# Performance work log

Hardware: AMD Instinct MI355X
Metric: run time of the kernel (lower is better)

Reference implementation:

```python
import jax, jax.numpy as jnp
import numpy as np

B, T, C, FREQ = 32, 512, 22, 192
HID = 128


def setup_inputs() -> dict:
    key = jax.random.key(0)
    k1, k2, k3, k4, k5, k6 = jax.random.split(key, 6)
    x = jax.random.normal(k1, (B, T, C, FREQ), dtype=jnp.float32)
    A = jax.random.uniform(k2, (B, T, C, C), dtype=jnp.float32)
    # Linear weights (torch layout: [out, in]); scaled like torch default init
    W0 = jax.random.normal(k3, (HID, FREQ), dtype=jnp.float32) / np.sqrt(FREQ)
    b0 = jax.random.normal(k4, (HID,), dtype=jnp.float32) * 0.01
    W1 = jax.random.normal(k5, (HID, HID), dtype=jnp.float32) / np.sqrt(HID)
    b1 = jax.random.normal(k6, (HID,), dtype=jnp.float32) * 0.01
    return {"x": x, "A": A, "W0": W0, "b0": b0, "W1": W1, "b1": b1}


def reference(x, A, W0, b0, W1, b1):
    # Vectorized over B and T simultaneously (original python-loops over t).
    # Layer i: xt = relu(Linear(bmm(A_t, xt)))
    h = x  # [B,T,C,Freq]
    for W, b in ((W0, b0), (W1, b1)):
        h = jnp.einsum('btij,btjf->btif', A, h)          # adjacency mix over nodes
        h = jax.nn.relu(jnp.einsum('btcf,hf->btch', h, W) + b)  # Linear + ReLU
    # stack over t is implicit; mean over node dim C -> [B,T,HID]
    return h.mean(axis=2)
```

## Files before the change

kernel.cpp:

```cpp
#include <hip/hip_runtime.h>

#define CC 22
#define FF 192
#define HH 128
#define NBT (32 * 512)

typedef __attribute__((ext_vector_type(8))) __bf16 bf16x8;
typedef __attribute__((ext_vector_type(8))) short s16x8;
typedef __attribute__((ext_vector_type(4))) float f32x4;

__device__ __forceinline__ float bf2f(unsigned short u) {
    union { unsigned int i; float f; } v;
    v.i = ((unsigned int)u) << 16;
    return v.f;
}

__device__ __forceinline__ unsigned short f2bf(float f) {
    union { float f; unsigned int i; } v;
    v.f = f;
    return (unsigned short)((v.i + 0x7fffu + ((v.i >> 16) & 1u)) >> 16);
}

__device__ __forceinline__ void split2(float v, unsigned short& h, unsigned short& l) {
    h = f2bf(v);
    float r = v - bf2f(h);
    l = f2bf(r);
}

__device__ __forceinline__ unsigned int cvt_pk_bf16(float a, float b) {
    unsigned int r;
    asm("v_cvt_pk_bf16_f32 %0, %1, %2" : "=v"(r) : "v"(a), "v"(b));
    return r;
}

__device__ __forceinline__ void split_pk2(float a, float b,
                                          unsigned int& hi, unsigned int& lo) {
    hi = cvt_pk_bf16(a, b);
    union { unsigned int i; float f; } ha, hb;
    ha.i = hi << 16;
    hb.i = hi & 0xffff0000u;
    lo = cvt_pk_bf16(a - ha.f, b - hb.f);
}

__device__ __forceinline__ bf16x8 bzero8() {
    s16x8 z = {0, 0, 0, 0, 0, 0, 0, 0};
    return __builtin_bit_cast(bf16x8, z);
}

__device__ __forceinline__ int ybyte(int row, int b) {
    return row * 64 + (b ^ (((row >> 1) & 3) << 4));
}

__device__ __forceinline__ int inputs_are_bf16(const unsigned short* __restrict__ A,
                                               int tid) {
    const float v = bf2f(A[tid & 63]);
    return __all(v >= 0.0f && v <= 1.0001f);
}

#define WS0H 0
#define WS0L 24576
#define WS1H 49152
#define WS1L 65536

__global__ void convert_weights(const float* __restrict__ W0g,
                                const float* __restrict__ W1g,
                                const unsigned short* __restrict__ Aany,
                                unsigned short* __restrict__ wsW) {
    if (inputs_are_bf16(Aany, threadIdx.x)) return;
    const int i = blockIdx.x * 256 + threadIdx.x;
    if (i < HH * FF) {
        unsigned short h, l;
        split2(W0g[i], h, l);
        wsW[WS0H + i] = h;
        wsW[WS0L + i] = l;
    } else {
        const int j = i - HH * FF;
        if (j < HH * HH) {
            unsigned short h, l;
            split2(W1g[j], h, l);
            wsW[WS1H + j] = h;
            wsW[WS1L + j] = l;
        }
    }
}

__device__ void run_block_f32(
    const float* __restrict__ xg, const float* __restrict__ Ag,
    const float* __restrict__ W0g, const float* __restrict__ b0g,
    const float* __restrict__ W1g, const float* __restrict__ b1g,
    float* __restrict__ outg, int bt, int tid,
    float* sA, float* sX, float* sH1)
{
    float* sH2  = sX;
    float* sH3  = sH1;
    float* sRed = sA;

    const float* Ap = Ag + (size_t)bt * (CC * CC);
    for (int i = tid; i < CC * CC; i += 256) sA[i] = Ap[i];
    const float4* xp = (const float4*)(xg + (size_t)bt * (CC * FF));
    for (int i = tid; i < CC * FF / 4; i += 256) ((float4*)sX)[i] = xp[i];
    __syncthreads();

    for (int idx4 = tid; idx4 < CC * FF / 4; idx4 += 256) {
        const int c  = idx4 / (FF / 4);
        const int fq = idx4 - c * (FF / 4);
        float4 acc = make_float4(0.f, 0.f, 0.f, 0.f);
        #pragma unroll
        for (int j = 0; j < CC; ++j) {
            const float  a  = sA[c * CC + j];
            const float4 xv = *(const float4*)&sX[j * FF + 4 * fq];
            acc.x += a * xv.x; acc.y += a * xv.y;
            acc.z += a * xv.z; acc.w += a * xv.w;
        }
        ((float4*)sH1)[idx4] = acc;
    }
    __syncthreads();

    const int h  = tid & 127;
    const int ty = tid >> 7;

    {
        float acc[11];
        const float bb = b0g[h];
        #pragma unroll
        for (int i = 0; i < 11; ++i) acc[i] = bb;
        #pragma unroll 4
        for (int fq = 0; fq < FF / 4; ++fq) {
            float4 u = ((const float4*)(W0g + h * FF))[fq];
            #pragma unroll
            for (int i = 0; i < 11; ++i) {
                const float4 xv = *(const float4*)&sH1[(2 * i + ty) * FF + 4 * fq];
                acc[i] = fmaf(xv.x, u.x, fmaf(xv.y, u.y, fmaf(xv.z, u.z, fmaf(xv.w, u.w, acc[i]))));
            }
        }
        #pragma unroll
        for (int i = 0; i < 11; ++i)
            sH2[(2 * i + ty) * HH + h] = fmaxf(acc[i], 0.f);
    }
    __syncthreads();

    for (int idx4 = tid; idx4 < CC * HH / 4; idx4 += 256) {
        const int c  = idx4 / (HH / 4);
        const int kq = idx4 - c * (HH / 4);
        float4 acc = make_float4(0.f, 0.f, 0.f, 0.f);
        #pragma unroll
        for (int j = 0; j < CC; ++j) {
            const float  a  = sA[c * CC + j];
            const float4 xv = *(const float4*)&sH2[j * HH + 4 * kq];
            acc.x += a * xv.x; acc.y += a * xv.y;
            acc.z += a * xv.z; acc.w += a * xv.w;
        }
        ((float4*)sH3)[idx4] = acc;
    }
    __syncthreads();

    {
        float acc[11];
        const float bb = b1g[h];
        #pragma unroll
        for (int i = 0; i < 11; ++i) acc[i] = bb;
        #pragma unroll 4
        for (int kq = 0; kq < HH / 4; ++kq) {
            float4 u = ((const float4*)(W1g + h * HH))[kq];
            #pragma unroll
            for (int i = 0; i < 11; ++i) {
                const float4 xv = *(const float4*)&sH3[(2 * i + ty) * HH + 4 * kq];
                acc[i] = fmaf(xv.x, u.x, fmaf(xv.y, u.y, fmaf(xv.z, u.z, fmaf(xv.w, u.w, acc[i]))));
            }
        }
        float s = 0.f;
        #pragma unroll
        for (int i = 0; i < 11; ++i) s += fmaxf(acc[i], 0.f);
        sRed[ty * HH + h] = s;
    }
    __syncthreads();

    if (ty == 0) {
        const float m = (sRed[h] + sRed[HH + h]) * (1.0f / 22.0f);
        outg[(size_t)bt * HH + h] = m;
    }
}

__device__ void run_block_split(
    const float* __restrict__ xg, const float* __restrict__ Ag,
    const float* __restrict__ b0g, const float* __restrict__ b1g,
    const unsigned short* __restrict__ wsW,
    float* __restrict__ outg, int bt, int tid, char* smem)
{
    unsigned short* sxh  = (unsigned short*)smem;
    unsigned short* sxl  = (unsigned short*)(smem + 8800);
    unsigned short* sAh  = (unsigned short*)(smem + 17600);
    unsigned short* sAl  = (unsigned short*)(smem + 20160);
    char*           syh  = smem + 22720;
    char*           syl  = smem + 30912;
    unsigned short* sh3h = (unsigned short*)smem;
    unsigned short* sh3l = (unsigned short*)(smem + 8704);

    const unsigned short* W0h = wsW + WS0H;
    const unsigned short* W0l = wsW + WS0L;
    const unsigned short* W1h = wsW + WS1H;
    const unsigned short* W1l = wsW + WS1L;

    {
        const float4* xp4 = (const float4*)(xg + (size_t)bt * (CC * FF));
        for (int idx = tid; idx < CC * (FF / 4); idx += 256) {
            const int c = idx / (FF / 4);
            const int q = idx - c * (FF / 4);
            const float4 v = xp4[idx];
            uint2 hv, lv;
            split_pk2(v.x, v.y, hv.x, lv.x);
            split_pk2(v.z, v.w, hv.y, lv.y);
            *(uint2*)&sxh[c * 200 + 4 * q] = hv;
            *(uint2*)&sxl[c * 200 + 4 * q] = lv;
        }
        const float* Ap = Ag + (size_t)bt * (CC * CC);
        for (int idx = tid; idx < 32 * 40; idx += 256) {
            const int r = idx / 40;
            const int c = idx - r * 40;
            unsigned short h = 0, l = 0;
            if (r < CC && c < CC) split2(Ap[r * CC + c], h, l);
            sAh[idx] = h;
            sAl[idx] = l;
        }
    }
    __syncthreads();

    const int lane = tid & 63;
    const int wid  = tid >> 6;
    const int lr   = lane & 15;
    const int lk   = lane >> 4;
    const int hb   = wid * 32;

    const f32x4 vzero = {0.f, 0.f, 0.f, 0.f};

    {
        f32x4 acc[2][2];
        #pragma unroll
        for (int mt = 0; mt < 2; ++mt)
            #pragma unroll
            for (int nt = 0; nt < 2; ++nt) acc[mt][nt] = vzero;

        #pragma unroll
        for (int ks = 0; ks < 6; ++ks) {
            bf16x8 xfh[2], xfl[2];
            #pragma unroll
            for (int mt = 0; mt < 2; ++mt) {
                const int row = mt * 16 + lr;
                const int rr  = (row < CC) ? row : 0;
                const int off = rr * 200 + ks * 32 + lk * 8;
                bf16x8 fh = *(const bf16x8*)(sxh + off);
                bf16x8 fl = *(const bf16x8*)(sxl + off);
                if (row >= CC) { fh = bzero8(); fl = bzero8(); }
                xfh[mt] = fh; xfl[mt] = fl;
            }
            bf16x8 wfh[2], wfl[2];
            #pragma unroll
            for (int nt = 0; nt < 2; ++nt) {
                const int hcol = hb + nt * 16 + lr;
                const int off  = hcol * FF + ks * 32 + lk * 8;
                wfh[nt] = *(const bf16x8*)(W0h + off);
                wfl[nt] = *(const bf16x8*)(W0l + off);
            }
            #pragma unroll
            for (int mt = 0; mt < 2; ++mt)
                #pragma unroll
                for (int nt = 0; nt < 2; ++nt) {
                    acc[mt][nt] = __builtin_amdgcn_mfma_f32_16x16x32_bf16(xfh[mt], wfh[nt], acc[mt][nt], 0, 0, 0);
                    acc[mt][nt] = __builtin_amdgcn_mfma_f32_16x16x32_bf16(xfl[mt], wfh[nt], acc[mt][nt], 0, 0, 0);
                    acc[mt][nt] = __builtin_amdgcn_mfma_f32_16x16x32_bf16(xfh[mt], wfl[nt], acc[mt][nt], 0, 0, 0);
                }
        }
        #pragma unroll
        for (int mt = 0; mt < 2; ++mt)
            #pragma unroll
            for (int nt = 0; nt < 2; ++nt) {
                const int hcol = hb + nt * 16 + lr;
                uint2 hv, lv;
                split_pk2(acc[mt][nt][0], acc[mt][nt][1], hv.x, lv.x);
                split_pk2(acc[mt][nt][2], acc[mt][nt][3], hv.y, lv.y);
                const int boff = ybyte(hcol, mt * 32 + lk * 8);
                *(uint2*)(syh + boff) = hv;
                *(uint2*)(syl + boff) = lv;
            }
    }
    __syncthreads();

    bf16x8 Afh[2], Afl[2];
    #pragma unroll
    for (int t = 0; t < 2; ++t) {
        const int off = (t * 16 + lr) * 40 + lk * 8;
        Afh[t] = *(const bf16x8*)(sAh + off);
        Afl[t] = *(const bf16x8*)(sAl + off);
    }

    {
        f32x4 acc[2][2];
        #pragma unroll
        for (int nt = 0; nt < 2; ++nt) {
            const float b = b0g[hb + nt * 16 + lr];
            const f32x4 bv = {b, b, b, b};
            acc[0][nt] = bv;
            acc[1][nt] = bv;
        }
        bf16x8 yfh[2], yfl[2];
        #pragma unroll
        for (int nt = 0; nt < 2; ++nt) {
            const int boff = ybyte(hb + nt * 16 + lr, lk * 16);
            yfh[nt] = *(const bf16x8*)(syh + boff);
            yfl[nt] = *(const bf16x8*)(syl + boff);
        }
        asm volatile("" ::: "memory");
        #pragma unroll
        for (int mt = 0; mt < 2; ++mt)
            #pragma unroll
            for (int nt = 0; nt < 2; ++nt) {
                acc[mt][nt] = __builtin_amdgcn_mfma_f32_16x16x32_bf16(Afh[mt], yfh[nt], acc[mt][nt], 0, 0, 0);
                acc[mt][nt] = __builtin_amdgcn_mfma_f32_16x16x32_bf16(Afl[mt], yfh[nt], acc[mt][nt], 0, 0, 0);
                acc[mt][nt] = __builtin_amdgcn_mfma_f32_16x16x32_bf16(Afh[mt], yfl[nt], acc[mt][nt], 0, 0, 0);
            }
        #pragma unroll
        for (int mt = 0; mt < 2; ++mt)
            #pragma unroll
            for (int nt = 0; nt < 2; ++nt) {
                const int hcol = hb + nt * 16 + lr;
                uint2 hv, lv;
                split_pk2(fmaxf(acc[mt][nt][0], 0.f), fmaxf(acc[mt][nt][1], 0.f), hv.x, lv.x);
                split_pk2(fmaxf(acc[mt][nt][2], 0.f), fmaxf(acc[mt][nt][3], 0.f), hv.y, lv.y);
                const int boff = ybyte(hcol, mt * 32 + lk * 8);
                *(uint2*)(syh + boff) = hv;
                *(uint2*)(syl + boff) = lv;
            }
    }

    {
        f32x4 acc[2][2];
        #pragma unroll
        for (int mt = 0; mt < 2; ++mt)
            #pragma unroll
            for (int ct = 0; ct < 2; ++ct) acc[mt][ct] = vzero;

        bf16x8 gfh[2], gfl[2];
        #pragma unroll
        for (int mt = 0; mt < 2; ++mt) {
            const int boff = ybyte(hb + mt * 16 + lr, lk * 16);
            gfh[mt] = *(const bf16x8*)(syh + boff);
            gfl[mt] = *(const bf16x8*)(syl + boff);
        }
        #pragma unroll
        for (int mt = 0; mt < 2; ++mt)
            #pragma unroll
            for (int ct = 0; ct < 2; ++ct) {
                acc[mt][ct] = __builtin_amdgcn_mfma_f32_16x16x32_bf16(gfh[mt], Afh[ct], acc[mt][ct], 0, 0, 0);
                acc[mt][ct] = __builtin_amdgcn_mfma_f32_16x16x32_bf16(gfl[mt], Afh[ct], acc[mt][ct], 0, 0, 0);
                acc[mt][ct] = __builtin_amdgcn_mfma_f32_16x16x32_bf16(gfh[mt], Afl[ct], acc[mt][ct], 0, 0, 0);
            }
        #pragma unroll
        for (int mt = 0; mt < 2; ++mt)
            #pragma unroll
            for (int ct = 0; ct < 2; ++ct) {
                const int cp = ct * 16 + lr;
                uint2 hv, lv;
                split_pk2(acc[mt][ct][0], acc[mt][ct][1], hv.x, lv.x);
                split_pk2(acc[mt][ct][2], acc[mt][ct][3], hv.y, lv.y);
                const int e = cp * 136 + hb + mt * 16 + lk * 4;
                *(uint2*)&sh3h[e] = hv;
                *(uint2*)&sh3l[e] = lv;
            }
    }
    __syncthreads();

    {
        f32x4 acc[2][2];
        #pragma unroll
        for (int mt = 0; mt < 2; ++mt) {
            const float4 bv = *(const float4*)(b1g + hb + mt * 16 + lk * 4);
            const f32x4 bb = {bv.x, bv.y, bv.z, bv.w};
            acc[mt][0] = bb;
            acc[mt][1] = bb;
        }
        #pragma unroll
        for (int ks = 0; ks < 4; ++ks) {
            bf16x8 wfh[2], wfl[2], hfh[2], hfl[2];
            #pragma unroll
            for (int mt = 0; mt < 2; ++mt) {
                const int o   = hb + mt * 16 + lr;
                const int off = o * HH + ks * 32 + lk * 8;
                wfh[mt] = *(const bf16x8*)(W1h + off);
                wfl[mt] = *(const bf16x8*)(W1l + off);
            }
            #pragma unroll
            for (int ct = 0; ct < 2; ++ct) {
                const int off = (ct * 16 + lr) * 136 + ks * 32 + lk * 8;
                hfh[ct] = *(const bf16x8*)(sh3h + off);
                hfl[ct] = *(const bf16x8*)(sh3l + off);
            }
            #pragma unroll
            for (int mt = 0; mt < 2; ++mt)
                #pragma unroll
                for (int ct = 0; ct < 2; ++ct) {
                    acc[mt][ct] = __builtin_amdgcn_mfma_f32_16x16x32_bf16(wfh[mt], hfh[ct], acc[mt][ct], 0, 0, 0);
                    acc[mt][ct] = __builtin_amdgcn_mfma_f32_16x16x32_bf16(wfl[mt], hfh[ct], acc[mt][ct], 0, 0, 0);
                    acc[mt][ct] = __builtin_amdgcn_mfma_f32_16x16x32_bf16(wfh[mt], hfl[ct], acc[mt][ct], 0, 0, 0);
                }
        }
        float s[2][4];
        #pragma unroll
        for (int mt = 0; mt < 2; ++mt)
            #pragma unroll
            for (int r = 0; r < 4; ++r) {
                float v = fmaxf(acc[mt][0][r], 0.f);
                if (lr < CC - 16) v += fmaxf(acc[mt][1][r], 0.f);
                s[mt][r] = v;
            }
        #pragma unroll
        for (int m = 1; m < 16; m <<= 1)
            #pragma unroll
            for (int mt = 0; mt < 2; ++mt)
                #pragma unroll
                for (int r = 0; r < 4; ++r)
                    s[mt][r] += __shfl_xor(s[mt][r], m);

        if (lr == 0) {
            const float inv = 1.0f / 22.0f;
            #pragma unroll
            for (int mt = 0; mt < 2; ++mt) {
                float4 o4;
                o4.x = s[mt][0] * inv;
                o4.y = s[mt][1] * inv;
                o4.z = s[mt][2] * inv;
                o4.w = s[mt][3] * inv;
                *(float4*)(outg + (size_t)bt * HH + hb + mt * 16 + lk * 4) = o4;
            }
        }
    }
}

__device__ void run_block_bf16(
    const unsigned short* __restrict__ xg, const unsigned short* __restrict__ Ag,
    const unsigned short* __restrict__ W0g, const unsigned short* __restrict__ b0g,
    const unsigned short* __restrict__ W1g, const unsigned short* __restrict__ b1g,
    unsigned short* __restrict__ outg, int bt, int tid, char* smem)
{
    unsigned short* sXT  = (unsigned short*)smem;
    unsigned short* sAm  = (unsigned short*)(smem + 15360);
    unsigned short* sH1  = (unsigned short*)(smem + 17920);
    unsigned short* sH2T = (unsigned short*)smem;
    unsigned short* sH3  = (unsigned short*)(smem + 17920);

    const unsigned short* xp = xg + (size_t)bt * (CC * FF);
    const unsigned short* Ap = Ag + (size_t)bt * (CC * CC);

    for (int id = tid; id < 32 * 40; id += 256) {
        const int r = id / 40;
        const int c = id - r * 40;
        sAm[id] = (r < CC && c < CC) ? Ap[r * CC + c] : (unsigned short)0;
    }
    for (int id = tid; id < FF * 9; id += 256) {
        const int f = id / 9;
        const int q = id - f * 9;
        ((unsigned int*)sXT)[f * 20 + 11 + q] = 0u;
    }
    for (int id = tid; id < 24 * CC; id += 256) {
        const int fb = id / CC;
        const int j  = id - fb * CC;
        const uint4 v = *(const uint4*)(xp + j * FF + fb * 8);
        unsigned short* d = sXT + (fb * 8) * 40 + j;
        d[0 * 40] = (unsigned short)(v.x & 0xffffu);
        d[1 * 40] = (unsigned short)(v.x >> 16);
        d[2 * 40] = (unsigned short)(v.y & 0xffffu);
        d[3 * 40] = (unsigned short)(v.y >> 16);
        d[4 * 40] = (unsigned short)(v.z & 0xffffu);
        d[5 * 40] = (unsigned short)(v.z >> 16);
        d[6 * 40] = (unsigned short)(v.w & 0xffffu);
        d[7 * 40] = (unsigned short)(v.w >> 16);
    }
    __syncthreads();

    const int lane = tid & 63;
    const int wid  = tid >> 6;
    const int lr   = lane & 15;
    const int lk   = lane >> 4;
    const f32x4 vzero = {0.f, 0.f, 0.f, 0.f};

    {
        f32x4 acc[3][2];
        #pragma unroll
        for (int i = 0; i < 3; ++i)
            #pragma unroll
            for (int j = 0; j < 2; ++j) acc[i][j] = vzero;
        bf16x8 xa[3], ab[2];
        #pragma unroll
        for (int i = 0; i < 3; ++i)
            xa[i] = *(const bf16x8*)(sXT + ((3 * wid + i) * 16 + lr) * 40 + lk * 8);
        #pragma unroll
        for (int j = 0; j < 2; ++j)
            ab[j] = *(const bf16x8*)(sAm + (j * 16 + lr) * 40 + lk * 8);
        #pragma unroll
        for (int i = 0; i < 3; ++i)
            #pragma unroll
            for (int j = 0; j < 2; ++j)
                acc[i][j] = __builtin_amdgcn_mfma_f32_16x16x32_bf16(xa[i], ab[j], acc[i][j], 0, 0, 0);
        #pragma unroll
        for (int i = 0; i < 3; ++i) {
            const int fbase = (3 * wid + i) * 16 + lk * 4;
            #pragma unroll
            for (int j = 0; j < 2; ++j) {
                const int c = j * 16 + lr;
                ushort4 st;
                st.x = f2bf(acc[i][j][0]);
                st.y = f2bf(acc[i][j][1]);
                st.z = f2bf(acc[i][j][2]);
                st.w = f2bf(acc[i][j][3]);
                *(ushort4*)(sH1 + c * 200 + fbase) = st;
            }
        }
    }
    __syncthreads();

    {
        f32x4 acc[2][2];
        #pragma unroll
        for (int nt = 0; nt < 2; ++nt) {
            const float bv = bf2f(b0g[(2 * wid + nt) * 16 + lr]);
            f32x4 bvv = {bv, bv, bv, bv};
            acc[0][nt] = bvv;
            acc[1][nt] = bvv;
        }
        #pragma unroll
        for (int ks = 0; ks < 6; ++ks) {
            bf16x8 af[2], bfr[2];
            #pragma unroll
            for (int mt = 0; mt < 2; ++mt)
                af[mt] = *(const bf16x8*)(sH1 + (mt * 16 + lr) * 200 + ks * 32 + lk * 8);
            #pragma unroll
            for (int nt = 0; nt < 2; ++nt)
                bfr[nt] = *(const bf16x8*)(W0g + ((size_t)((2 * wid + nt) * 16 + lr)) * FF + ks * 32 + lk * 8);
            #pragma unroll
            for (int mt = 0; mt < 2; ++mt)
                #pragma unroll
                for (int nt = 0; nt < 2; ++nt)
                    acc[mt][nt] = __builtin_amdgcn_mfma_f32_16x16x32_bf16(af[mt], bfr[nt], acc[mt][nt], 0, 0, 0);
        }
        #pragma unroll
        for (int mt = 0; mt < 2; ++mt) {
            const int cbase = mt * 16 + lk * 4;
            #pragma unroll
            for (int nt = 0; nt < 2; ++nt) {
                const int hcol = (2 * wid + nt) * 16 + lr;
                ushort4 st;
                st.x = (cbase + 0 < CC) ? f2bf(fmaxf(acc[mt][nt][0], 0.f)) : (unsigned short)0;
                st.y = (cbase + 1 < CC) ? f2bf(fmaxf(acc[mt][nt][1], 0.f)) : (unsigned short)0;
                st.z = (cbase + 2 < CC) ? f2bf(fmaxf(acc[mt][nt][2], 0.f)) : (unsigned short)0;
                st.w = (cbase + 3 < CC) ? f2bf(fmaxf(acc[mt][nt][3], 0.f)) : (unsigned short)0;
                *(ushort4*)(sH2T + hcol * 40 + cbase) = st;
            }
        }
    }
    __syncthreads();

    {
        f32x4 acc[2][2];
        #pragma unroll
        for (int mt = 0; mt < 2; ++mt)
            #pragma unroll
            for (int ct = 0; ct < 2; ++ct) acc[mt][ct] = vzero;
        bf16x8 af[2], bb[2];
        #pragma unroll
        for (int mt = 0; mt < 2; ++mt)
            af[mt] = *(const bf16x8*)(sH2T + ((2 * wid + mt) * 16 + lr) * 40 + lk * 8);
        #pragma unroll
        for (int ct = 0; ct < 2; ++ct)
            bb[ct] = *(const bf16x8*)(sAm + (ct * 16 + lr) * 40 + lk * 8);
        #pragma unroll
        for (int mt = 0; mt < 2; ++mt)
            #pragma unroll
            for (int ct = 0; ct < 2; ++ct)
                acc[mt][ct] = __builtin_amdgcn_mfma_f32_16x16x32_bf16(af[mt], bb[ct], acc[mt][ct], 0, 0, 0);
        __syncthreads();
        #pragma unroll
        for (int mt = 0; mt < 2; ++mt) {
            const int hbase = (2 * wid + mt) * 16 + lk * 4;
            #pragma unroll
            for (int ct = 0; ct < 2; ++ct) {
                const int c = ct * 16 + lr;
                ushort4 st;
                st.x = f2bf(acc[mt][ct][0]);
                st.y = f2bf(acc[mt][ct][1]);
                st.z = f2bf(acc[mt][ct][2]);
                st.w = f2bf(acc[mt][ct][3]);
                *(ushort4*)(sH3 + c * 136 + hbase) = st;
            }
        }
    }
    __syncthreads();

    {
        f32x4 acc[2][2];
        #pragma unroll
        for (int mt = 0; mt < 2; ++mt) {
            const ushort4 bu = *(const ushort4*)(b1g + (2 * wid + mt) * 16 + lk * 4);
            f32x4 bvv = {bf2f(bu.x), bf2f(bu.y), bf2f(bu.z), bf2f(bu.w)};
            acc[mt][0] = bvv;
            acc[mt][1] = bvv;
        }
        #pragma unroll
        for (int ks = 0; ks < 4; ++ks) {
            bf16x8 af[2], bfr[2];
            #pragma unroll
            for (int mt = 0; mt < 2; ++mt)
                af[mt] = *(const bf16x8*)(W1g + ((size_t)((2 * wid + mt) * 16 + lr)) * HH + ks * 32 + lk * 8);
            #pragma unroll
            for (int ct = 0; ct < 2; ++ct)
                bfr[ct] = *(const bf16x8*)(sH3 + (ct * 16 + lr) * 136 + ks * 32 + lk * 8);
            #pragma unroll
            for (int mt = 0; mt < 2; ++mt)
                #pragma unroll
                for (int ct = 0; ct < 2; ++ct)
                    acc[mt][ct] = __builtin_amdgcn_mfma_f32_16x16x32_bf16(af[mt], bfr[ct], acc[mt][ct], 0, 0, 0);
        }
        float s[2][4];
        #pragma unroll
        for (int mt = 0; mt < 2; ++mt)
            #pragma unroll
            for (int r = 0; r < 4; ++r) {
                float v = fmaxf(acc[mt][0][r], 0.f);
                if (lr < CC - 16) v += fmaxf(acc[mt][1][r], 0.f);
                s[mt][r] = v;
            }
        #pragma unroll
        for (int m = 1; m < 16; m <<= 1)
            #pragma unroll
            for (int mt = 0; mt < 2; ++mt)
                #pragma unroll
                for (int r = 0; r < 4; ++r)
                    s[mt][r] += __shfl_xor(s[mt][r], m);
        if (lr == 0) {
            const float inv = 1.0f / 22.0f;
            #pragma unroll
            for (int mt = 0; mt < 2; ++mt) {
                ushort4 st;
                st.x = f2bf(s[mt][0] * inv);
                st.y = f2bf(s[mt][1] * inv);
                st.z = f2bf(s[mt][2] * inv);
                st.w = f2bf(s[mt][3] * inv);
                *(ushort4*)(outg + (size_t)bt * HH + (2 * wid + mt) * 16 + lk * 4) = st;
            }
        }
    }
}

__global__ __launch_bounds__(256) void tgcn_kernel(
    const void* __restrict__ x, const void* __restrict__ A,
    const void* __restrict__ W0, const void* __restrict__ b0,
    const void* __restrict__ W1, const void* __restrict__ b1,
    void* __restrict__ out, const unsigned short* __restrict__ wsW,
    int use_split)
{
    __shared__ __align__(16) char smem[39104];

    const int tid = threadIdx.x;
    const int bt  = blockIdx.x;
    const int isbf = inputs_are_bf16((const unsigned short*)A, tid);

    if (isbf) {
        run_block_bf16((const unsigned short*)x, (const unsigned short*)A,
                       (const unsigned short*)W0, (const unsigned short*)b0,
                       (const unsigned short*)W1, (const unsigned short*)b1,
                       (unsigned short*)out, bt, tid, smem);
    } else if (use_split) {
        run_block_split((const float*)x, (const float*)A,
                        (const float*)b0, (const float*)b1,
                        wsW, (float*)out, bt, tid, smem);
    } else {
        float* sA  = (float*)smem;
        float* sX  = (float*)(smem + 1936);
        float* sH1 = (float*)(smem + 18832);
        run_block_f32((const float*)x, (const float*)A,
                      (const float*)W0, (const float*)b0,
                      (const float*)W1, (const float*)b1,
                      (float*)out, bt, tid, sA, sX, sH1);
    }
}

extern "C" void kernel_launch(void* const* d_in, const int* in_sizes, int n_in,
                              void* d_out, int out_size, void* d_ws, size_t ws_size,
                              hipStream_t stream) {
    unsigned short* wsW = (unsigned short*)d_ws;
    const int use_split = (ws_size >= (size_t)(81920 * 2)) ? 1 : 0;

    if (use_split)
        convert_weights<<<160, 256, 0, stream>>>(
            (const float*)d_in[2], (const float*)d_in[4],
            (const unsigned short*)d_in[1], wsW);
    tgcn_kernel<<<NBT, 256, 0, stream>>>(
        d_in[0], d_in[1], d_in[2], d_in[3], d_in[4], d_in[5], d_out,
        wsW, use_split);
}
```

Before: 701.7 us.

## Reorder to project features first, split fp32 inputs in registers, drop weight prepass

The fp32 split path now loads x and the weights straight from global memory and splits them into bf16 hi/lo pairs in registers. This removes the shared-memory staging of x and the separate weight-conversion kernel and workspace. The bf16 path is reordered to apply W0 before the adjacency mix (A(xW)=(Ax)W), which shrinks the first mix from 192 to 128 features and removes the transposed x staging. Shared memory per block drops, which may raise occupancy. In exchange, every block repeats the weight split arithmetic and reads uncoalesced fp32 weights from global memory, and the reordering changes rounding.

Result: slower. 722.8 us (+3.0%).

```diff
diff --git a/kernel.cpp b/kernel.cpp
--- a/kernel.cpp
+++ b/kernel.cpp
@@ -42,6 +42,19 @@
     lo = cvt_pk_bf16(a - ha.f, b - hb.f);
 }
 
+__device__ __forceinline__ void load_split8(const float* __restrict__ p,
+                                            bf16x8& fh, bf16x8& fl) {
+    const float4 a = *(const float4*)p;
+    const float4 b = *(const float4*)(p + 4);
+    uint4 h, l;
+    split_pk2(a.x, a.y, h.x, l.x);
+    split_pk2(a.z, a.w, h.y, l.y);
+    split_pk2(b.x, b.y, h.z, l.z);
+    split_pk2(b.z, b.w, h.w, l.w);
+    fh = __builtin_bit_cast(bf16x8, h);
+    fl = __builtin_bit_cast(bf16x8, l);
+}
+
 __device__ __forceinline__ bf16x8 bzero8() {
     s16x8 z = {0, 0, 0, 0, 0, 0, 0, 0};
     return __builtin_bit_cast(bf16x8, z);
@@ -57,162 +70,20 @@
     return __all(v >= 0.0f && v <= 1.0001f);
 }
 
-#define WS0H 0
-#define WS0L 24576
-#define WS1H 49152
-#define WS1L 65536
-
-__global__ void convert_weights(const float* __restrict__ W0g,
-                                const float* __restrict__ W1g,
-                                const unsigned short* __restrict__ Aany,
-                                unsigned short* __restrict__ wsW) {
-    if (inputs_are_bf16(Aany, threadIdx.x)) return;
-    const int i = blockIdx.x * 256 + threadIdx.x;
-    if (i < HH * FF) {
-        unsigned short h, l;
-        split2(W0g[i], h, l);
-        wsW[WS0H + i] = h;
-        wsW[WS0L + i] = l;
-    } else {
-        const int j = i - HH * FF;
-        if (j < HH * HH) {
-            unsigned short h, l;
-            split2(W1g[j], h, l);
-            wsW[WS1H + j] = h;
-            wsW[WS1L + j] = l;
-        }
-    }
-}
-
-__device__ void run_block_f32(
+__device__ void run_block_split(
     const float* __restrict__ xg, const float* __restrict__ Ag,
     const float* __restrict__ W0g, const float* __restrict__ b0g,
     const float* __restrict__ W1g, const float* __restrict__ b1g,
-    float* __restrict__ outg, int bt, int tid,
-    float* sA, float* sX, float* sH1)
-{
-    float* sH2  = sX;
-    float* sH3  = sH1;
-    float* sRed = sA;
-
-    const float* Ap = Ag + (size_t)bt * (CC * CC);
-    for (int i = tid; i < CC * CC; i += 256) sA[i] = Ap[i];
-    const float4* xp = (const float4*)(xg + (size_t)bt * (CC * FF));
-    for (int i = tid; i < CC * FF / 4; i += 256) ((float4*)sX)[i] = xp[i];
-    __syncthreads();
-
-    for (int idx4 = tid; idx4 < CC * FF / 4; idx4 += 256) {
-        const int c  = idx4 / (FF / 4);
-        const int fq = idx4 - c * (FF / 4);
-        float4 acc = make_float4(0.f, 0.f, 0.f, 0.f);
-        #pragma unroll
-        for (int j = 0; j < CC; ++j) {
-            const float  a  = sA[c * CC + j];
-            const float4 xv = *(const float4*)&sX[j * FF + 4 * fq];
-            acc.x += a * xv.x; acc.y += a * xv.y;
-            acc.z += a * xv.z; acc.w += a * xv.w;
-        }
-        ((float4*)sH1)[idx4] = acc;
-    }
-    __syncthreads();
-
-    const int h  = tid & 127;
-    const int ty = tid >> 7;
-
-    {
-        float acc[11];
-        const float bb = b0g[h];
-        #pragma unroll
-        for (int i = 0; i < 11; ++i) acc[i] = bb;
-        #pragma unroll 4
-        for (int fq = 0; fq < FF / 4; ++fq) {
-            float4 u = ((const float4*)(W0g + h * FF))[fq];
-            #pragma unroll
-            for (int i = 0; i < 11; ++i) {
-                const float4 xv = *(const float4*)&sH1[(2 * i + ty) * FF + 4 * fq];
-                acc[i] = fmaf(xv.x, u.x, fmaf(xv.y, u.y, fmaf(xv.z, u.z, fmaf(xv.w, u.w, acc[i]))));
-            }
-        }
-        #pragma unroll
-        for (int i = 0; i < 11; ++i)
-            sH2[(2 * i + ty) * HH + h] = fmaxf(acc[i], 0.f);
-    }
-    __syncthreads();
-
-    for (int idx4 = tid; idx4 < CC * HH / 4; idx4 += 256) {
-        const int c  = idx4 / (HH / 4);
-        const int kq = idx4 - c * (HH / 4);
-        float4 acc = make_float4(0.f, 0.f, 0.f, 0.f);
-        #pragma unroll
-        for (int j = 0; j < CC; ++j) {
-            const float  a  = sA[c * CC + j];
-            const float4 xv = *(const float4*)&sH2[j * HH + 4 * kq];
-            acc.x += a * xv.x; acc.y += a * xv.y;
-            acc.z += a * xv.z; acc.w += a * xv.w;
-        }
-        ((float4*)sH3)[idx4] = acc;
-    }
-    __syncthreads();
-
-    {
-        float acc[11];
-        const float bb = b1g[h];
-        #pragma unroll
-        for (int i = 0; i < 11; ++i) acc[i] = bb;
-        #pragma unroll 4
-        for (int kq = 0; kq < HH / 4; ++kq) {
-            float4 u = ((const float4*)(W1g + h * HH))[kq];
-            #pragma unroll
-            for (int i = 0; i < 11; ++i) {
-                const float4 xv = *(const float4*)&sH3[(2 * i + ty) * HH + 4 * kq];
-                acc[i] = fmaf(xv.x, u.x, fmaf(xv.y, u.y, fmaf(xv.z, u.z, fmaf(xv.w, u.w, acc[i]))));
-            }
-        }
-        float s = 0.f;
-        #pragma unroll
-        for (int i = 0; i < 11; ++i) s += fmaxf(acc[i], 0.f);
-        sRed[ty * HH + h] = s;
-    }
-    __syncthreads();
-
-    if (ty == 0) {
-        const float m = (sRed[h] + sRed[HH + h]) * (1.0f / 22.0f);
-        outg[(size_t)bt * HH + h] = m;
-    }
-}
-
-__device__ void run_block_split(
-    const float* __restrict__ xg, const float* __restrict__ Ag,
-    const float* __restrict__ b0g, const float* __restrict__ b1g,
-    const unsigned short* __restrict__ wsW,
     float* __restrict__ outg, int bt, int tid, char* smem)
 {
-    unsigned short* sxh  = (unsigned short*)smem;
-    unsigned short* sxl  = (unsigned short*)(smem + 8800);
-    unsigned short* sAh  = (unsigned short*)(smem + 17600);
-    unsigned short* sAl  = (unsigned short*)(smem + 20160);
-    char*           syh  = smem + 22720;
-    char*           syl  = smem + 30912;
+    unsigned short* sAh  = (unsigned short*)smem;
+    unsigned short* sAl  = (unsigned short*)(smem + 2560);
+    char*           syh  = smem + 5120;
+    char*           syl  = smem + 13312;
     unsigned short* sh3h = (unsigned short*)smem;
     unsigned short* sh3l = (unsigned short*)(smem + 8704);
 
-    const unsigned short* W0h = wsW + WS0H;
-    const unsigned short* W0l = wsW + WS0L;
-    const unsigned short* W1h = wsW + WS1H;
-    const unsigned short* W1l = wsW + WS1L;
-
-    {
-        const float4* xp4 = (const float4*)(xg + (size_t)bt * (CC * FF));
-        for (int idx = tid; idx < CC * (FF / 4); idx += 256) {
-            const int c = idx / (FF / 4);
-            const int q = idx - c * (FF / 4);
-            const float4 v = xp4[idx];
-            uint2 hv, lv;
-            split_pk2(v.x, v.y, hv.x, lv.x);
-            split_pk2(v.z, v.w, hv.y, lv.y);
-            *(uint2*)&sxh[c * 200 + 4 * q] = hv;
-            *(uint2*)&sxl[c * 200 + 4 * q] = lv;
-        }
+    {
         const float* Ap = Ag + (size_t)bt * (CC * CC);
         for (int idx = tid; idx < 32 * 40; idx += 256) {
             const int r = idx / 40;
@@ -233,7 +104,16 @@
 
     const f32x4 vzero = {0.f, 0.f, 0.f, 0.f};
 
-    {
+    bf16x8 Afh[2], Afl[2];
+    #pragma unroll
+    for (int t = 0; t < 2; ++t) {
+        const int off = (t * 16 + lr) * 40 + lk * 8;
+        Afh[t] = *(const bf16x8*)(sAh + off);
+        Afl[t] = *(const bf16x8*)(sAl + off);
+    }
+
+    {
+        const float* xb = xg + (size_t)bt * (CC * FF);
         f32x4 acc[2][2];
         #pragma unroll
         for (int mt = 0; mt < 2; ++mt)
@@ -247,9 +127,8 @@
             for (int mt = 0; mt < 2; ++mt) {
                 const int row = mt * 16 + lr;
                 const int rr  = (row < CC) ? row : 0;
-                const int off = rr * 200 + ks * 32 + lk * 8;
-                bf16x8 fh = *(const bf16x8*)(sxh + off);
-                bf16x8 fl = *(const bf16x8*)(sxl + off);
+                bf16x8 fh, fl;
+                load_split8(xb + rr * FF + ks * 32 + lk * 8, fh, fl);
                 if (row >= CC) { fh = bzero8(); fl = bzero8(); }
                 xfh[mt] = fh; xfl[mt] = fl;
             }
@@ -257,9 +136,7 @@
             #pragma unroll
             for (int nt = 0; nt < 2; ++nt) {
                 const int hcol = hb + nt * 16 + lr;
-                const int off  = hcol * FF + ks * 32 + lk * 8;
-                wfh[nt] = *(const bf16x8*)(W0h + off);
-                wfl[nt] = *(const bf16x8*)(W0l + off);
+                load_split8(W0g + hcol * FF + ks * 32 + lk * 8, wfh[nt], wfl[nt]);
             }
             #pragma unroll
             for (int mt = 0; mt < 2; ++mt)
@@ -283,15 +160,6 @@
                 *(uint2*)(syl + boff) = lv;
             }
     }
-    __syncthreads();
-
-    bf16x8 Afh[2], Afl[2];
-    #pragma unroll
-    for (int t = 0; t < 2; ++t) {
-        const int off = (t * 16 + lr) * 40 + lk * 8;
-        Afh[t] = *(const bf16x8*)(sAh + off);
-        Afl[t] = *(const bf16x8*)(sAl + off);
-    }
 
     {
         f32x4 acc[2][2];
@@ -354,6 +222,7 @@
                 acc[mt][ct] = __builtin_amdgcn_mfma_f32_16x16x32_bf16(gfl[mt], Afh[ct], acc[mt][ct], 0, 0, 0);
                 acc[mt][ct] = __builtin_amdgcn_mfma_f32_16x16x32_bf16(gfh[mt], Afl[ct], acc[mt][ct], 0, 0, 0);
             }
+        __syncthreads();
         #pragma unroll
         for (int mt = 0; mt < 2; ++mt)
             #pragma unroll
@@ -383,10 +252,8 @@
             bf16x8 wfh[2], wfl[2], hfh[2], hfl[2];
             #pragma unroll
             for (int mt = 0; mt < 2; ++mt) {
-                const int o   = hb + mt * 16 + lr;
-                const int off = o * HH + ks * 32 + lk * 8;
-                wfh[mt] = *(const bf16x8*)(W1h + off);
-                wfl[mt] = *(const bf16x8*)(W1l + off);
+                const int o = hb + mt * 16 + lr;
+                load_split8(W1g + o * HH + ks * 32 + lk * 8, wfh[mt], wfl[mt]);
             }
             #pragma unroll
             for (int ct = 0; ct < 2; ++ct) {
@@ -441,38 +308,17 @@
     const unsigned short* __restrict__ W1g, const unsigned short* __restrict__ b1g,
     unsigned short* __restrict__ outg, int bt, int tid, char* smem)
 {
-    unsigned short* sXT  = (unsigned short*)smem;
-    unsigned short* sAm  = (unsigned short*)(smem + 15360);
-    unsigned short* sH1  = (unsigned short*)(smem + 17920);
-    unsigned short* sH2T = (unsigned short*)smem;
-    unsigned short* sH3  = (unsigned short*)(smem + 17920);
-
-    const unsigned short* xp = xg + (size_t)bt * (CC * FF);
-    const unsigned short* Ap = Ag + (size_t)bt * (CC * CC);
-
-    for (int id = tid; id < 32 * 40; id += 256) {
-        const int r = id / 40;
-        const int c = id - r * 40;
-        sAm[id] = (r < CC && c < CC) ? Ap[r * CC + c] : (unsigned short)0;
-    }
-    for (int id = tid; id < FF * 9; id += 256) {
-        const int f = id / 9;
-        const int q = id - f * 9;
-        ((unsigned int*)sXT)[f * 20 + 11 + q] = 0u;
-    }
-    for (int id = tid; id < 24 * CC; id += 256) {
-        const int fb = id / CC;
-        const int j  = id - fb * CC;
-        const uint4 v = *(const uint4*)(xp + j * FF + fb * 8);
-        unsigned short* d = sXT + (fb * 8) * 40 + j;
-        d[0 * 40] = (unsigned short)(v.x & 0xffffu);
-        d[1 * 40] = (unsigned short)(v.x >> 16);
-        d[2 * 40] = (unsigned short)(v.y & 0xffffu);
-        d[3 * 40] = (unsigned short)(v.y >> 16);
-        d[4 * 40] = (unsigned short)(v.z & 0xffffu);
-        d[5 * 40] = (unsigned short)(v.z >> 16);
-        d[6 * 40] = (unsigned short)(v.w & 0xffffu);
-        d[7 * 40] = (unsigned short)(v.w >> 16);
+    unsigned short* sAm = (unsigned short*)smem;
+    char*           sy  = smem + 2560;
+    unsigned short* sh3 = (unsigned short*)smem;
+
+    {
+        const unsigned short* Ap = Ag + (size_t)bt * (CC * CC);
+        for (int idx = tid; idx < 32 * 40; idx += 256) {
+            const int r = idx / 40;
+            const int c = idx - r * 40;
+            sAm[idx] = (r < CC && c < CC) ? Ap[r * CC + c] : (unsigned short)0;
+        }
     }
     __syncthreads();
 
@@ -480,143 +326,136 @@
     const int wid  = tid >> 6;
     const int lr   = lane & 15;
     const int lk   = lane >> 4;
+    const int hb   = wid * 32;
     const f32x4 vzero = {0.f, 0.f, 0.f, 0.f};
 
-    {
-        f32x4 acc[3][2];
-        #pragma unroll
-        for (int i = 0; i < 3; ++i)
-            #pragma unroll
-            for (int j = 0; j < 2; ++j) acc[i][j] = vzero;
-        bf16x8 xa[3], ab[2];
-        #pragma unroll
-        for (int i = 0; i < 3; ++i)
-            xa[i] = *(const bf16x8*)(sXT + ((3 * wid + i) * 16 + lr) * 40 + lk * 8);
-        #pragma unroll
-        for (int j = 0; j < 2; ++j)
-            ab[j] = *(const bf16x8*)(sAm + (j * 16 + lr) * 40 + lk * 8);
-        #pragma unroll
-        for (int i = 0; i < 3; ++i)
-            #pragma unroll
-            for (int j = 0; j < 2; ++j)
-                acc[i][j] = __builtin_amdgcn_mfma_f32_16x16x32_bf16(xa[i], ab[j], acc[i][j], 0, 0, 0);
-        #pragma unroll
-        for (int i = 0; i < 3; ++i) {
-            const int fbase = (3 * wid + i) * 16 + lk * 4;
-            #pragma unroll
-            for (int j = 0; j < 2; ++j) {
-                const int c = j * 16 + lr;
-                ushort4 st;
-                st.x = f2bf(acc[i][j][0]);
-                st.y = f2bf(acc[i][j][1]);
-                st.z = f2bf(acc[i][j][2]);
-                st.w = f2bf(acc[i][j][3]);
-                *(ushort4*)(sH1 + c * 200 + fbase) = st;
-            }
-        }
-    }
-    __syncthreads();
-
-    {
-        f32x4 acc[2][2];
-        #pragma unroll
-        for (int nt = 0; nt < 2; ++nt) {
-            const float bv = bf2f(b0g[(2 * wid + nt) * 16 + lr]);
-            f32x4 bvv = {bv, bv, bv, bv};
-            acc[0][nt] = bvv;
-            acc[1][nt] = bvv;
-        }
+    bf16x8 Af[2];
+    #pragma unroll
+    for (int t = 0; t < 2; ++t)
+        Af[t] = *(const bf16x8*)(sAm + (t * 16 + lr) * 40 + lk * 8);
+
+    {
+        const unsigned short* xb = xg + (size_t)bt * (CC * FF);
+        f32x4 acc[2][2];
+        #pragma unroll
+        for (int mt = 0; mt < 2; ++mt)
+            #pragma unroll
+            for (int nt = 0; nt < 2; ++nt) acc[mt][nt] = vzero;
         #pragma unroll
         for (int ks = 0; ks < 6; ++ks) {
-            bf16x8 af[2], bfr[2];
-            #pragma unroll
-            for (int mt = 0; mt < 2; ++mt)
-                af[mt] = *(const bf16x8*)(sH1 + (mt * 16 + lr) * 200 + ks * 32 + lk * 8);
+            bf16x8 xf[2], wf[2];
+            #pragma unroll
+            for (int mt = 0; mt < 2; ++mt) {
+                const int row = mt * 16 + lr;
+                const int rr  = (row < CC) ? row : 0;
+                bf16x8 f = *(const bf16x8*)(xb + rr * FF + ks * 32 + lk * 8);
+                if (row >= CC) f = bzero8();
+                xf[mt] = f;
+            }
             #pragma unroll
             for (int nt = 0; nt < 2; ++nt)
-                bfr[nt] = *(const bf16x8*)(W0g + ((size_t)((2 * wid + nt) * 16 + lr)) * FF + ks * 32 + lk * 8);
+                wf[nt] = *(const bf16x8*)(W0g + ((size_t)(hb + nt * 16 + lr)) * FF + ks * 32 + lk * 8);
             #pragma unroll
             for (int mt = 0; mt < 2; ++mt)
                 #pragma unroll
                 for (int nt = 0; nt < 2; ++nt)
-                    acc[mt][nt] = __builtin_amdgcn_mfma_f32_16x16x32_bf16(af[mt], bfr[nt], acc[mt][nt], 0, 0, 0);
-        }
+                    acc[mt][nt] = __builtin_amdgcn_mfma_f32_16x16x32_bf16(xf[mt], wf[nt], acc[mt][nt], 0, 0, 0);
+        }
+        #pragma unroll
+        for (int mt = 0; mt < 2; ++mt)
+            #pragma unroll
+            for (int nt = 0; nt < 2; ++nt) {
+                const int hcol = hb + nt * 16 + lr;
+                uint2 hv;
+                hv.x = cvt_pk_bf16(acc[mt][nt][0], acc[mt][nt][1]);
+                hv.y = cvt_pk_bf16(acc[mt][nt][2], acc[mt][nt][3]);
+                *(uint2*)(sy + ybyte(hcol, mt * 32 + lk * 8)) = hv;
+            }
+    }
+
+    {
+        f32x4 acc[2][2];
+        #pragma unroll
+        for (int nt = 0; nt < 2; ++nt) {
+            const float b = bf2f(b0g[hb + nt * 16 + lr]);
+            const f32x4 bv = {b, b, b, b};
+            acc[0][nt] = bv;
+            acc[1][nt] = bv;
+        }
+        bf16x8 yf[2];
+        #pragma unroll
+        for (int nt = 0; nt < 2; ++nt)
+            yf[nt] = *(const bf16x8*)(sy + ybyte(hb + nt * 16 + lr, lk * 16));
+        asm volatile("" ::: "memory");
+        #pragma unroll
+        for (int mt = 0; mt < 2; ++mt)
+            #pragma unroll
+            for (int nt = 0; nt < 2; ++nt)
+                acc[mt][nt] = __builtin_amdgcn_mfma_f32_16x16x32_bf16(Af[mt], yf[nt], acc[mt][nt], 0, 0, 0);
+        #pragma unroll
+        for (int mt = 0; mt < 2; ++mt)
+            #pragma unroll
+            for (int nt = 0; nt < 2; ++nt) {
+                const int hcol = hb + nt * 16 + lr;
+                uint2 hv;
+                hv.x = cvt_pk_bf16(fmaxf(acc[mt][nt][0], 0.f), fmaxf(acc[mt][nt][1], 0.f));
+                hv.y = cvt_pk_bf16(fmaxf(acc[mt][nt][2], 0.f), fmaxf(acc[mt][nt][3], 0.f));
+                *(uint2*)(sy + ybyte(hcol, mt * 32 + lk * 8)) = hv;
+            }
+    }
+
+    {
+        f32x4 acc[2][2];
+        #pragma unroll
+        for (int mt = 0; mt < 2; ++mt)
+            #pragma unroll
+            for (int ct = 0; ct < 2; ++ct) acc[mt][ct] = vzero;
+        bf16x8 gf[2];
+        #pragma unroll
+        for (int mt = 0; mt < 2; ++mt)
+            gf[mt] = *(const bf16x8*)(sy + ybyte(hb + mt * 16 + lr, lk * 16));
+        #pragma unroll
+        for (int mt = 0; mt < 2; ++mt)
+            #pragma unroll
+            for (int ct = 0; ct < 2; ++ct)
+                acc[mt][ct] = __builtin_amdgcn_mfma_f32_16x16x32_bf16(gf[mt], Af[ct], acc[mt][ct], 0, 0, 0);
+        __syncthreads();
+        #pragma unroll
+        for (int mt = 0; mt < 2; ++mt)
+            #pragma unroll
+            for (int ct = 0; ct < 2; ++ct) {
+                const int cp = ct * 16 + lr;
+                uint2 hv;
+                hv.x = cvt_pk_bf16(acc[mt][ct][0], acc[mt][ct][1]);
+                hv.y = cvt_pk_bf16(acc[mt][ct][2], acc[mt][ct][3]);
+                *(uint2*)&sh3[cp * 136 + hb + mt * 16 + lk * 4] = hv;
+            }
+    }
+    __syncthreads();
+
+    {
+        f32x4 acc[2][2];
         #pragma unroll
         for (int mt = 0; mt < 2; ++mt) {
-            const int cbase = mt * 16 + lk * 4;
-            #pragma unroll
-            for (int nt = 0; nt < 2; ++nt) {
-                const int hcol = (2 * wid + nt) * 16 + lr;
-                ushort4 st;
-                st.x = (cbase + 0 < CC) ? f2bf(fmaxf(acc[mt][nt][0], 0.f)) : (unsigned short)0;
-                st.y = (cbase + 1 < CC) ? f2bf(fmaxf(acc[mt][nt][1], 0.f)) : (unsigned short)0;
-                st.z = (cbase + 2 < CC) ? f2bf(fmaxf(acc[mt][nt][2], 0.f)) : (unsigned short)0;
-                st.w = (cbase + 3 < CC) ? f2bf(fmaxf(acc[mt][nt][3], 0.f)) : (unsigned short)0;
-                *(ushort4*)(sH2T + hcol * 40 + cbase) = st;
-            }
-        }
-    }
-    __syncthreads();
-
-    {
-        f32x4 acc[2][2];
-        #pragma unroll
-        for (int mt = 0; mt < 2; ++mt)
-            #pragma unroll
-            for (int ct = 0; ct < 2; ++ct) acc[mt][ct] = vzero;
-        bf16x8 af[2], bb[2];
-        #pragma unroll
-        for (int mt = 0; mt < 2; ++mt)
-            af[mt] = *(const bf16x8*)(sH2T + ((2 * wid + mt) * 16 + lr) * 40 + lk * 8);
-        #pragma unroll
-        for (int ct = 0; ct < 2; ++ct)
-            bb[ct] = *(const bf16x8*)(sAm + (ct * 16 + lr) * 40 + lk * 8);
-        #pragma unroll
-        for (int mt = 0; mt < 2; ++mt)
-            #pragma unroll
-            for (int ct = 0; ct < 2; ++ct)
-                acc[mt][ct] = __builtin_amdgcn_mfma_f32_16x16x32_bf16(af[mt], bb[ct], acc[mt][ct], 0, 0, 0);
-        __syncthreads();
-        #pragma unroll
-        for (int mt = 0; mt < 2; ++mt) {
-            const int hbase = (2 * wid + mt) * 16 + lk * 4;
-            #pragma unroll
-            for (int ct = 0; ct < 2; ++ct) {
-                const int c = ct * 16 + lr;
-                ushort4 st;
-                st.x = f2bf(acc[mt][ct][0]);
-                st.y = f2bf(acc[mt][ct][1]);
-                st.z = f2bf(acc[mt][ct][2]);
-                st.w = f2bf(acc[mt][ct][3]);
-                *(ushort4*)(sH3 + c * 136 + hbase) = st;
-            }
-        }
-    }
-    __syncthreads();
-
-    {
-        f32x4 acc[2][2];
-        #pragma unroll
-        for (int mt = 0; mt < 2; ++mt) {
-            const ushort4 bu = *(const ushort4*)(b1g + (2 * wid + mt) * 16 + lk * 4);
+            const ushort4 bu = *(const ushort4*)(b1g + hb + mt * 16 + lk * 4);
             f32x4 bvv = {bf2f(bu.x), bf2f(bu.y), bf2f(bu.z), bf2f(bu.w)};
             acc[mt][0] = bvv;
             acc[mt][1] = bvv;
         }
         #pragma unroll
         for (int ks = 0; ks < 4; ++ks) {
-            bf16x8 af[2], bfr[2];
-            #pragma unroll
-            for (int mt = 0; mt < 2; ++mt)
-                af[mt] = *(const bf16x8*)(W1g + ((size_t)((2 * wid + mt) * 16 + lr)) * HH + ks * 32 + lk * 8);
+            bf16x8 wf[2], hf[2];
+            #pragma unroll
+            for (int mt = 0; mt < 2; ++mt)
+                wf[mt] = *(const bf16x8*)(W1g + ((size_t)(hb + mt * 16 + lr)) * HH + ks * 32 + lk * 8);
             #pragma unroll
             for (int ct = 0; ct < 2; ++ct)
-                bfr[ct] = *(const bf16x8*)(sH3 + (ct * 16 + lr) * 136 + ks * 32 + lk * 8);
+                hf[ct] = *(const bf16x8*)(sh3 + (ct * 16 + lr) * 136 + ks * 32 + lk * 8);
             #pragma unroll
             for (int mt = 0; mt < 2; ++mt)
                 #pragma unroll
                 for (int ct = 0; ct < 2; ++ct)
-                    acc[mt][ct] = __builtin_amdgcn_mfma_f32_16x16x32_bf16(af[mt], bfr[ct], acc[mt][ct], 0, 0, 0);
+                    acc[mt][ct] = __builtin_amdgcn_mfma_f32_16x16x32_bf16(wf[mt], hf[ct], acc[mt][ct], 0, 0, 0);
         }
         float s[2][4];
         #pragma unroll
@@ -638,12 +477,10 @@
             const float inv = 1.0f / 22.0f;
             #pragma unroll
             for (int mt = 0; mt < 2; ++mt) {
-                ushort4 st;
-                st.x = f2bf(s[mt][0] * inv);
-                st.y = f2bf(s[mt][1] * inv);
-                st.z = f2bf(s[mt][2] * inv);
-                st.w = f2bf(s[mt][3] * inv);
-                *(ushort4*)(outg + (size_t)bt * HH + (2 * wid + mt) * 16 + lk * 4) = st;
+                uint2 st;
+                st.x = cvt_pk_bf16(s[mt][0] * inv, s[mt][1] * inv);
+                st.y = cvt_pk_bf16(s[mt][2] * inv, s[mt][3] * inv);
+                *(uint2*)(outg + (size_t)bt * HH + hb + mt * 16 + lk * 4) = st;
             }
         }
     }
@@ -653,10 +490,9 @@
     const void* __restrict__ x, const void* __restrict__ A,
     const void* __restrict__ W0, const void* __restrict__ b0,
     const void* __restrict__ W1, const void* __restrict__ b1,
-    void* __restrict__ out, const unsigned short* __restrict__ wsW,
-    int use_split)
+    void* __restrict__ out)
 {
-    __shared__ __align__(16) char smem[39104];
+    __shared__ __align__(16) char smem[21504];
 
     const int tid = threadIdx.x;
     const int bt  = blockIdx.x;
@@ -667,32 +503,17 @@
                        (const unsigned short*)W0, (const unsigned short*)b0,
                        (const unsigned short*)W1, (const unsigned short*)b1,
                        (unsigned short*)out, bt, tid, smem);
-    } else if (use_split) {
+    } else {
         run_block_split((const float*)x, (const float*)A,
-                        (const float*)b0, (const float*)b1,
-                        wsW, (float*)out, bt, tid, smem);
-    } else {
-        float* sA  = (float*)smem;
-        float* sX  = (float*)(smem + 1936);
-        float* sH1 = (float*)(smem + 18832);
-        run_block_f32((const float*)x, (const float*)A,
-                      (const float*)W0, (const float*)b0,
-                      (const float*)W1, (const float*)b1,
-                      (float*)out, bt, tid, sA, sX, sH1);
+                        (const float*)W0, (const float*)b0,
+                        (const float*)W1, (const float*)b1,
+                        (float*)out, bt, tid, smem);
     }
 }
 
 extern "C" void kernel_launch(void* const* d_in, const int* in_sizes, int n_in,
                               void* d_out, int out_size, void* d_ws, size_t ws_size,
                               hipStream_t stream) {
-    unsigned short* wsW = (unsigned short*)d_ws;
-    const int use_split = (ws_size >= (size_t)(81920 * 2)) ? 1 : 0;
-
-    if (use_split)
-        convert_weights<<<160, 256, 0, stream>>>(
-            (const float*)d_in[2], (const float*)d_in[4],
-            (const unsigned short*)d_in[1], wsW);
     tgcn_kernel<<<NBT, 256, 0, stream>>>(
-        d_in[0], d_in[1], d_in[2], d_in[3], d_in[4], d_in[5], d_out,
-        wsW, use_split);
-}
+        d_in[0], d_in[1], d_in[2], d_in[3], d_in[4], d_in[5], d_out);
+}
```
